# Kernel tuning notes

Hardware: AMD Instinct MI355X
Metric: run time of the kernel (lower is better)

## Reference

```python
import jax, jax.numpy as jnp
import numpy as np

HEADS = 8  # head_num from init_kwargs


def setup_inputs() -> dict:
    key = jax.random.key(0)
    k1, k2, k3 = jax.random.split(key, 3)
    x = jax.random.normal(k1, (1, 512, 16, 16, 16), dtype=jnp.float32)
    # 1x1x1 Conv3d kernels are pointwise linear maps over channels
    w_qkv = jax.random.normal(k2, (1536, 512), dtype=jnp.float32) * 0.02
    w_out = jax.random.normal(k3, (512, 512), dtype=jnp.float32) * 0.02
    return {"x": x, "w_qkv": w_qkv, "w_out": w_out}


def reference(x, w_qkv, w_out):
    B, C, D, H, W = x.shape
    h = HEADS
    dh = C // h
    scale = float(dh) ** 0.5  # NOTE: source MULTIPLIES by sqrt(dh) (dk), faithful here
    N = D * H * W

    # pointwise Conv3d == per-token linear: [B, N, C]
    xt = x.reshape(B, C, N).transpose(0, 2, 1)
    qkv = xt @ w_qkv.T                                   # [B, N, 3C]
    qkv = qkv.reshape(B, N, 3, h, dh).transpose(2, 0, 3, 1, 4)  # [3, B, h, N, dh]
    q, k, v = qkv[0], qkv[1], qkv[2]

    energy = jnp.einsum('bhid,bhjd->bhij', q, k) * scale  # [B, h, N, N]
    attn = jax.nn.softmax(energy, axis=-1)
    o = jnp.einsum('bhij,bhjd->bhid', attn, v)            # [B, h, N, dh]

    o = o.transpose(0, 2, 1, 3).reshape(B, N, C)          # [B, N, C]
    out = o @ w_out.T                                     # [B, N, C]
    return out.transpose(0, 2, 1).reshape(B, C, D, H, W)
```

## Files before the change

### kernel.cpp

```cpp
#include <hip/hip_runtime.h>

typedef unsigned short u16;
typedef unsigned int u32;
typedef unsigned long long u64;
typedef __bf16 bf16x8 __attribute__((ext_vector_type(8)));
typedef float f32x4 __attribute__((ext_vector_type(4)));
typedef u16 u16x8 __attribute__((ext_vector_type(8)));

#define C_DIM 512
#define N_TOK 4096
#define HEADS 8
#define K3 1536
#define QSCALE 11.5415603071f

__device__ __forceinline__ u16 f2bf(float f) {
  u32 u = __builtin_bit_cast(u32, f);
  u += 0x7FFFu + ((u >> 16) & 1u);
  return (u16)(u >> 16);
}
__device__ __forceinline__ float bf2f(u16 b) {
  u32 u = ((u32)b) << 16;
  return __builtin_bit_cast(float, u);
}

__global__ void prep_w_kernel(const float* __restrict__ w, u16* __restrict__ A1) {
  int i = blockIdx.x * 256 + threadIdx.x;
  if (i >= 1536 * 512) return;
  int m = i >> 9, c = i & 511;
  float v = w[i];
  u16 hi = f2bf(v);
  u16 lo = f2bf(v - bf2f(hi));
  u16* row = A1 + (size_t)m * K3;
  row[c] = hi; row[512 + c] = hi; row[1024 + c] = lo;
}

__global__ void prep_wout_kernel(const float* __restrict__ w, u16* __restrict__ A2) {
  int i = blockIdx.x * 256 + threadIdx.x;
  if (i >= 512 * 512) return;
  A2[i] = f2bf(w[i]);
}

__global__ __launch_bounds__(256) void prep_x_kernel(const float* __restrict__ x, u16* __restrict__ B1) {
  __shared__ float lds[64][65];
  int n0 = blockIdx.x * 64, c0 = blockIdx.y * 64;
  int tid = threadIdx.x;
#pragma unroll
  for (int i = 0; i < 4; i++) {
    int idx = tid + i * 256;
    int r = idx >> 4, s = idx & 15;
    const float4 v = *(const float4*)(x + (size_t)(c0 + r) * N_TOK + n0 + s * 4);
    lds[r][s * 4 + 0] = v.x; lds[r][s * 4 + 1] = v.y;
    lds[r][s * 4 + 2] = v.z; lds[r][s * 4 + 3] = v.w;
  }
  __syncthreads();
  int n = tid >> 2, cs = tid & 3;
  u16x8 hv[2], lv[2];
#pragma unroll
  for (int half = 0; half < 2; half++) {
#pragma unroll
    for (int j = 0; j < 8; j++) {
      float v = lds[cs * 16 + half * 8 + j][n];
      u16 hi = f2bf(v);
      hv[half][j] = hi;
      lv[half][j] = f2bf(v - bf2f(hi));
    }
  }
  u16* row = B1 + (size_t)(n0 + n) * K3 + c0 + cs * 16;
  *(u16x8*)(row) = hv[0];
  *(u16x8*)(row + 8) = hv[1];
  *(u16x8*)(row + 512) = lv[0];
  *(u16x8*)(row + 520) = lv[1];
  *(u16x8*)(row + 1024) = hv[0];
  *(u16x8*)(row + 1032) = hv[1];
}

__global__ __launch_bounds__(256) void gemm_nt_kernel(
    const u16* __restrict__ A, const u16* __restrict__ B, float* __restrict__ C,
    int M, int N, int K) {
  __shared__ char lds[128 * 64 * 2 * 2];
  char* ldsA = lds;
  char* ldsB = lds + 128 * 64 * 2;
  int n0 = blockIdx.x * 128, m0 = blockIdx.y * 128;
  int tid = threadIdx.x, lane = tid & 63, wid = tid >> 6;
  int wr = wid >> 1, wc = wid & 1;
  f32x4 acc[4][4] = {};
  for (int k0 = 0; k0 < K; k0 += 64) {
    __syncthreads();
#pragma unroll
    for (int i = 0; i < 4; i++) {
      int idx = tid + i * 256;
      int row = idx >> 3, cb = idx & 7;
      uint4 va = *(const uint4*)(A + (size_t)(m0 + row) * K + k0 + cb * 8);
      *(uint4*)(ldsA + row * 128 + ((cb * 16) ^ ((row & 7) << 4))) = va;
      uint4 vb = *(const uint4*)(B + (size_t)(n0 + row) * K + k0 + cb * 8);
      *(uint4*)(ldsB + row * 128 + ((cb * 16) ^ ((row & 7) << 4))) = vb;
    }
    __syncthreads();
#pragma unroll
    for (int kk = 0; kk < 2; kk++) {
      bf16x8 af[4], bfr[4];
#pragma unroll
      for (int mt = 0; mt < 4; mt++) {
        int row = wr * 64 + mt * 16 + (lane & 15);
        int kb = kk * 64 + ((lane >> 4) << 4);
        af[mt] = *(const bf16x8*)(ldsA + row * 128 + (kb ^ ((row & 7) << 4)));
      }
#pragma unroll
      for (int nt = 0; nt < 4; nt++) {
        int row = wc * 64 + nt * 16 + (lane & 15);
        int kb = kk * 64 + ((lane >> 4) << 4);
        bfr[nt] = *(const bf16x8*)(ldsB + row * 128 + (kb ^ ((row & 7) << 4)));
      }
#pragma unroll
      for (int mt = 0; mt < 4; mt++)
#pragma unroll
        for (int nt = 0; nt < 4; nt++)
          acc[mt][nt] = __builtin_amdgcn_mfma_f32_16x16x32_bf16(af[mt], bfr[nt], acc[mt][nt], 0, 0, 0);
    }
  }
#pragma unroll
  for (int mt = 0; mt < 4; mt++)
#pragma unroll
    for (int nt = 0; nt < 4; nt++) {
      int row = m0 + wr * 64 + mt * 16 + ((lane >> 4) << 2);
      int col = n0 + wc * 64 + nt * 16 + (lane & 15);
#pragma unroll
      for (int r = 0; r < 4; r++)
        C[(size_t)(row + r) * N + col] = acc[mt][nt][r];
    }
}

__global__ void prep_qk_kernel(const float* __restrict__ qkv, u16* __restrict__ Qp, u16* __restrict__ Kp) {
  int i = blockIdx.x * 256 + threadIdx.x;
  int dh = i & 63;
  int n = (i >> 6) & 4095;
  int h = i >> 18;
  float q = qkv[(size_t)n * K3 + h * 64 + dh] * QSCALE;
  float k = qkv[(size_t)n * K3 + 512 + h * 64 + dh];
  u16 qhi = f2bf(q); u16 qlo = f2bf(q - bf2f(qhi));
  u16 khi = f2bf(k); u16 klo = f2bf(k - bf2f(khi));
  u16* qr = Qp + ((size_t)h * N_TOK + n) * 128;
  u16* kr = Kp + ((size_t)h * N_TOK + n) * 128;
  qr[dh] = qhi; qr[64 + dh] = qlo;
  kr[dh] = khi; kr[64 + dh] = klo;
}

__global__ __launch_bounds__(256) void prep_v_kernel(const float* __restrict__ qkv, u16* __restrict__ Vt) {
  __shared__ float lds[64][65];
  int n0 = blockIdx.x * 64, h = blockIdx.y;
  int tid = threadIdx.x;
#pragma unroll
  for (int i = 0; i < 4; i++) {
    int idx = tid + i * 256;
    int r = idx >> 4, s = idx & 15;
    const float4 v = *(const float4*)(qkv + (size_t)(n0 + r) * K3 + 1024 + h * 64 + s * 4);
    lds[r][s * 4 + 0] = v.x; lds[r][s * 4 + 1] = v.y;
    lds[r][s * 4 + 2] = v.z; lds[r][s * 4 + 3] = v.w;
  }
  __syncthreads();
  int dh = tid >> 2, ns = tid & 3;
  u16x8 pv[2];
#pragma unroll
  for (int half = 0; half < 2; half++)
#pragma unroll
    for (int j = 0; j < 8; j++)
      pv[half][j] = f2bf(lds[ns * 16 + half * 8 + j][dh]);
  u16* dst = Vt + ((size_t)h * 64 + dh) * N_TOK + n0 + ns * 16;
  *(u16x8*)(dst) = pv[0];
  *(u16x8*)(dst + 8) = pv[1];
}

__global__ __launch_bounds__(256) void attn_kernel(
    const u16* __restrict__ Qp, const u16* __restrict__ Kp,
    const u16* __restrict__ Vt, float* __restrict__ Uws,
    float* __restrict__ Mws, float* __restrict__ Lws) {
  __shared__ char lds[32768];
  char* ldsK = lds;
  char* ldsV = lds + 16384;
  char* ldsP = lds + 24576;
  int bid = blockIdx.x;
  int h = bid & 7;
  int rest = bid >> 3;
  int half = rest & 1;
  int q0 = (rest >> 1) * 64;
  int kvbase = half * 2048;
  int tid = threadIdx.x, lane = tid & 63, wid = tid >> 6;
  char* myP = ldsP + wid * 2048;
  int qcol = lane & 15;
  int g = lane >> 4;

  bf16x8 qf[4];
  {
    const u16* qrow = Qp + ((size_t)h * N_TOK + q0 + wid * 16 + qcol) * 128 + (g * 8);
#pragma unroll
    for (int c = 0; c < 4; c++) qf[c] = *(const bf16x8*)(qrow + c * 32);
  }
  const u16* Kbase = Kp + (size_t)h * N_TOK * 128;
  const u16* Vbase = Vt + (size_t)h * 64 * N_TOK;

  f32x4 o[4] = {};
  float mrow = -INFINITY, lrow = 0.f;

  for (int t = 0; t < 32; ++t) {
    int kv0 = kvbase + t * 64;
    __syncthreads();
#pragma unroll
    for (int i = 0; i < 4; i++) {
      int idx = tid + i * 256, row = idx >> 4, cb = idx & 15;
      uint4 v = *(const uint4*)(Kbase + (size_t)(kv0 + row) * 128 + cb * 8);
      *(uint4*)(ldsK + row * 256 + ((cb * 16) ^ ((row & 7) << 4))) = v;
    }
#pragma unroll
    for (int i = 0; i < 2; i++) {
      int idx = tid + i * 256, row = idx >> 3, cb = idx & 7;
      uint4 v = *(const uint4*)(Vbase + (size_t)row * N_TOK + kv0 + cb * 8);
      *(uint4*)(ldsV + row * 128 + ((cb * 16) ^ ((row & 7) << 4))) = v;
    }
    __syncthreads();

    f32x4 s[4];
#pragma unroll
    for (int nt = 0; nt < 4; nt++) {
      int row = nt * 16 + qcol;
      const char* kb = ldsK + row * 256;
      int swz = (row & 7) << 4;
      int ko = g << 4;
      bf16x8 kf0 = *(const bf16x8*)(kb + ((ko) ^ swz));
      bf16x8 kf1 = *(const bf16x8*)(kb + ((64 + ko) ^ swz));
      bf16x8 kf2 = *(const bf16x8*)(kb + ((128 + ko) ^ swz));
      bf16x8 kf3 = *(const bf16x8*)(kb + ((192 + ko) ^ swz));
      f32x4 acc = {};
      acc = __builtin_amdgcn_mfma_f32_16x16x32_bf16(kf0, qf[0], acc, 0, 0, 0);
      acc = __builtin_amdgcn_mfma_f32_16x16x32_bf16(kf1, qf[1], acc, 0, 0, 0);
      acc = __builtin_amdgcn_mfma_f32_16x16x32_bf16(kf2, qf[0], acc, 0, 0, 0);
      acc = __builtin_amdgcn_mfma_f32_16x16x32_bf16(kf3, qf[1], acc, 0, 0, 0);
      acc = __builtin_amdgcn_mfma_f32_16x16x32_bf16(kf0, qf[2], acc, 0, 0, 0);
      acc = __builtin_amdgcn_mfma_f32_16x16x32_bf16(kf1, qf[3], acc, 0, 0, 0);
      s[nt] = acc;
    }

    float m = s[0][0];
#pragma unroll
    for (int nt = 0; nt < 4; nt++)
#pragma unroll
      for (int r = 0; r < 4; r++) m = fmaxf(m, s[nt][r]);
    m = fmaxf(m, __shfl_xor(m, 16));
    m = fmaxf(m, __shfl_xor(m, 32));
    float mnew = fmaxf(mrow, m);
    float alpha = exp2f(mrow - mnew);
    mrow = mnew;
    float psum = 0.f;
#pragma unroll
    for (int nt = 0; nt < 4; nt++)
#pragma unroll
      for (int r = 0; r < 4; r++) {
        float p = exp2f(s[nt][r] - mnew);
        s[nt][r] = p;
        psum += p;
      }
    psum += __shfl_xor(psum, 16);
    psum += __shfl_xor(psum, 32);
    lrow = lrow * alpha + psum;

#pragma unroll
    for (int r = 0; r < 4; r++) {
      float a = __shfl(alpha, (g << 2) | r);
      o[0][r] *= a; o[1][r] *= a; o[2][r] *= a; o[3][r] *= a;
    }

#pragma unroll
    for (int nt = 0; nt < 4; nt++) {
      u16 h0 = f2bf(s[nt][0]), h1 = f2bf(s[nt][1]);
      u16 h2 = f2bf(s[nt][2]), h3 = f2bf(s[nt][3]);
      u32 w0 = (u32)h0 | ((u32)h1 << 16);
      u32 w1 = (u32)h2 | ((u32)h3 << 16);
      int off = (nt * 32 + g * 8) ^ ((qcol & 7) << 4);
      *(uint2*)(myP + qcol * 128 + off) = make_uint2(w0, w1);
    }

#pragma unroll
    for (int c = 0; c < 2; c++) {
      int prow = lane & 15;
      int kb2 = c * 64 + (g << 4);
      bf16x8 pf = *(const bf16x8*)(myP + prow * 128 + (kb2 ^ ((prow & 7) << 4)));
#pragma unroll
      for (int nt = 0; nt < 4; nt++) {
        int vrow = nt * 16 + (lane & 15);
        bf16x8 vf = *(const bf16x8*)(ldsV + vrow * 128 + (kb2 ^ ((vrow & 7) << 4)));
        o[nt] = __builtin_amdgcn_mfma_f32_16x16x32_bf16(pf, vf, o[nt], 0, 0, 0);
      }
    }
  }

  size_t base = ((size_t)(half * HEADS + h) * N_TOK);
#pragma unroll
  for (int r = 0; r < 4; r++) {
    int tok = q0 + wid * 16 + (g << 2) + r;
    float* urow = Uws + (base + tok) * 64;
#pragma unroll
    for (int nt = 0; nt < 4; nt++)
      urow[nt * 16 + (lane & 15)] = o[nt][r];
  }
  if (g == 0) {
    int tok = q0 + wid * 16 + qcol;
    Mws[base + tok] = mrow;
    Lws[base + tok] = lrow;
  }
}

__global__ void reduce_kernel(const float* __restrict__ Uws, const float* __restrict__ Mws,
                              const float* __restrict__ Lws, u16* __restrict__ Obuf) {
  int i = blockIdx.x * 256 + threadIdx.x;
  int d4 = i & 15;
  int tok = (i >> 4) & 4095;
  int h = i >> 16;
  size_t b1 = (size_t)h * N_TOK + tok;
  size_t b2 = (size_t)(HEADS + h) * N_TOK + tok;
  float m1 = Mws[b1], m2 = Mws[b2];
  float l1 = Lws[b1], l2 = Lws[b2];
  float m = fmaxf(m1, m2);
  float w1 = exp2f(m1 - m), w2 = exp2f(m2 - m);
  float inv = 1.0f / (l1 * w1 + l2 * w2);
  f32x4 u1 = *(const f32x4*)(Uws + b1 * 64 + d4 * 4);
  f32x4 u2 = *(const f32x4*)(Uws + b2 * 64 + d4 * 4);
  u16* dst = Obuf + (size_t)tok * C_DIM + h * 64 + d4 * 4;
#pragma unroll
  for (int j = 0; j < 4; j++)
    dst[j] = f2bf((u1[j] * w1 + u2[j] * w2) * inv);
}

extern "C" void kernel_launch(void* const* d_in, const int* in_sizes, int n_in,
                              void* d_out, int out_size, void* d_ws, size_t ws_size,
                              hipStream_t stream) {
  const float* x = (const float*)d_in[0];
  const float* w_qkv = (const float*)d_in[1];
  const float* w_out = (const float*)d_in[2];
  float* out = (float*)d_out;
  char* ws = (char*)d_ws;
  size_t off = 0;
  size_t off_B1 = off;  off += (size_t)N_TOK * K3 * 2;
  size_t off_A1 = off;  off += (size_t)K3 * K3 * 2;
  size_t off_A2 = off;  off += (size_t)512 * 512 * 2;
  size_t off_qkv = off; off += (size_t)N_TOK * K3 * 4;
  size_t off_Qp = off;  off += (size_t)HEADS * N_TOK * 128 * 2;
  size_t off_Kp = off;  off += (size_t)HEADS * N_TOK * 128 * 2;
  u16* B1 = (u16*)(ws + off_B1);
  u16* A1 = (u16*)(ws + off_A1);
  u16* A2 = (u16*)(ws + off_A2);
  float* qkv = (float*)(ws + off_qkv);
  u16* Qp = (u16*)(ws + off_Qp);
  u16* Kp = (u16*)(ws + off_Kp);
  u16* Vt = (u16*)(ws + off_A1);
  u16* Obuf = (u16*)(ws + off_B1);
  float* Uws = (float*)(ws + off_qkv);
  float* Mws = (float*)(ws + off_qkv + 16777216);
  float* Lws = (float*)(ws + off_qkv + 16777216 + 262144);

  prep_w_kernel<<<(1536 * 512 + 255) / 256, 256, 0, stream>>>(w_qkv, A1);
  prep_wout_kernel<<<(512 * 512 + 255) / 256, 256, 0, stream>>>(w_out, A2);
  prep_x_kernel<<<dim3(64, 8), 256, 0, stream>>>(x, B1);
  gemm_nt_kernel<<<dim3(K3 / 128, N_TOK / 128), 256, 0, stream>>>(B1, A1, qkv, N_TOK, K3, K3);
  prep_qk_kernel<<<(HEADS * N_TOK * 64) / 256, 256, 0, stream>>>(qkv, Qp, Kp);
  prep_v_kernel<<<dim3(64, 8), 256, 0, stream>>>(qkv, Vt);
  attn_kernel<<<1024, 256, 0, stream>>>(Qp, Kp, Vt, Uws, Mws, Lws);
  reduce_kernel<<<(HEADS * N_TOK * 16) / 256, 256, 0, stream>>>(Uws, Mws, Lws, Obuf);
  gemm_nt_kernel<<<dim3(N_TOK / 128, 512 / 128), 256, 0, stream>>>(A2, Obuf, out, 512, N_TOK, 512);
}
```

Baseline: 235.5 us.

## Pre-swizzle K/V tiles and double-buffer attention loads via global_load_lds

The prep kernels now write K and V into pre-swizzled per-tile images that match the attention kernel's LDS layout. This lets the attention kernel copy tiles straight from global memory into LDS with global_load_lds, bypassing registers. K/V tiles are double-buffered so the next tile's load overlaps current compute, cutting one barrier per iteration. LDS offsets are precomputed and s_setprio is raised around MFMA blocks; the costs are more LDS per block (lower occupancy) and scattered 2-byte writes in prep_qk.

Result: slower. 255.4 us (+8.5%).

```diff
diff --git a/kernel.cpp b/kernel.cpp
--- a/kernel.cpp
+++ b/kernel.cpp
@@ -12,6 +12,11 @@
 #define HEADS 8
 #define K3 1536
 #define QSCALE 11.5415603071f
+
+#define GLDS(SRC, DST)                                                        \
+  __builtin_amdgcn_global_load_lds(                                           \
+      (const __attribute__((address_space(1))) void*)(SRC),                   \
+      (__attribute__((address_space(3))) void*)(DST), 16, 0, 0)
 
 __device__ __forceinline__ u16 f2bf(float f) {
   u32 u = __builtin_bit_cast(u32, f);
@@ -56,13 +61,13 @@
   int n = tid >> 2, cs = tid & 3;
   u16x8 hv[2], lv[2];
 #pragma unroll
-  for (int half = 0; half < 2; half++) {
+  for (int half2 = 0; half2 < 2; half2++) {
 #pragma unroll
     for (int j = 0; j < 8; j++) {
-      float v = lds[cs * 16 + half * 8 + j][n];
+      float v = lds[cs * 16 + half2 * 8 + j][n];
       u16 hi = f2bf(v);
-      hv[half][j] = hi;
-      lv[half][j] = f2bf(v - bf2f(hi));
+      hv[half2][j] = hi;
+      lv[half2][j] = f2bf(v - bf2f(hi));
     }
   }
   u16* row = B1 + (size_t)(n0 + n) * K3 + c0 + cs * 16;
@@ -130,7 +135,7 @@
     }
 }
 
-__global__ void prep_qk_kernel(const float* __restrict__ qkv, u16* __restrict__ Qp, u16* __restrict__ Kp) {
+__global__ void prep_qk_kernel(const float* __restrict__ qkv, u16* __restrict__ Qp, u16* __restrict__ Kimg) {
   int i = blockIdx.x * 256 + threadIdx.x;
   int dh = i & 63;
   int n = (i >> 6) & 4095;
@@ -140,14 +145,20 @@
   u16 qhi = f2bf(q); u16 qlo = f2bf(q - bf2f(qhi));
   u16 khi = f2bf(k); u16 klo = f2bf(k - bf2f(khi));
   u16* qr = Qp + ((size_t)h * N_TOK + n) * 128;
-  u16* kr = Kp + ((size_t)h * N_TOK + n) * 128;
   qr[dh] = qhi; qr[64 + dh] = qlo;
-  kr[dh] = khi; kr[64 + dh] = klo;
-}
-
-__global__ __launch_bounds__(256) void prep_v_kernel(const float* __restrict__ qkv, u16* __restrict__ Vt) {
+  u16* kt = Kimg + ((size_t)h * 64 + (n >> 6)) * 8192;
+  int row = n & 63;
+  int swz = (row & 7) << 4;
+  int bh = row * 256 + (((dh >> 3) * 16) ^ swz);
+  int bl = row * 256 + ((((dh >> 3) + 8) * 16) ^ swz);
+  kt[(bh >> 1) + (dh & 7)] = khi;
+  kt[(bl >> 1) + (dh & 7)] = klo;
+}
+
+__global__ __launch_bounds__(256) void prep_v_kernel(const float* __restrict__ qkv, u16* __restrict__ Vimg) {
   __shared__ float lds[64][65];
-  int n0 = blockIdx.x * 64, h = blockIdx.y;
+  int tile = blockIdx.x, h = blockIdx.y;
+  int n0 = tile * 64;
   int tid = threadIdx.x;
 #pragma unroll
   for (int i = 0; i < 4; i++) {
@@ -159,33 +170,31 @@
   }
   __syncthreads();
   int dh = tid >> 2, ns = tid & 3;
-  u16x8 pv[2];
-#pragma unroll
-  for (int half = 0; half < 2; half++)
+  u16* vt = Vimg + ((size_t)h * 64 + tile) * 4096;
+#pragma unroll
+  for (int half2 = 0; half2 < 2; half2++) {
+    u16x8 pv;
 #pragma unroll
     for (int j = 0; j < 8; j++)
-      pv[half][j] = f2bf(lds[ns * 16 + half * 8 + j][dh]);
-  u16* dst = Vt + ((size_t)h * 64 + dh) * N_TOK + n0 + ns * 16;
-  *(u16x8*)(dst) = pv[0];
-  *(u16x8*)(dst + 8) = pv[1];
+      pv[j] = f2bf(lds[ns * 16 + half2 * 8 + j][dh]);
+    int cb = ns * 2 + half2;
+    int off = dh * 64 + ((((cb * 16) ^ ((dh & 7) << 4))) >> 1);
+    *(u16x8*)(vt + off) = pv;
+  }
 }
 
 __global__ __launch_bounds__(256) void attn_kernel(
-    const u16* __restrict__ Qp, const u16* __restrict__ Kp,
-    const u16* __restrict__ Vt, float* __restrict__ Uws,
+    const u16* __restrict__ Qp, const u16* __restrict__ Kimg,
+    const u16* __restrict__ Vimg, float* __restrict__ Uws,
     float* __restrict__ Mws, float* __restrict__ Lws) {
-  __shared__ char lds[32768];
-  char* ldsK = lds;
-  char* ldsV = lds + 16384;
-  char* ldsP = lds + 24576;
+  __shared__ char lds[57344];
   int bid = blockIdx.x;
   int h = bid & 7;
   int rest = bid >> 3;
   int half = rest & 1;
   int q0 = (rest >> 1) * 64;
-  int kvbase = half * 2048;
   int tid = threadIdx.x, lane = tid & 63, wid = tid >> 6;
-  char* myP = ldsP + wid * 2048;
+  char* myP = lds + 49152 + wid * 2048;
   int qcol = lane & 15;
   int g = lane >> 4;
 
@@ -195,40 +204,63 @@
 #pragma unroll
     for (int c = 0; c < 4; c++) qf[c] = *(const bf16x8*)(qrow + c * 32);
   }
-  const u16* Kbase = Kp + (size_t)h * N_TOK * 128;
-  const u16* Vbase = Vt + (size_t)h * 64 * N_TOK;
+
+  const char* ksrc = (const char*)Kimg + ((size_t)h * 64 + half * 32) * 16384 + wid * 1024 + lane * 16;
+  const char* vsrc = (const char*)Vimg + ((size_t)h * 64 + half * 32) * 8192 + wid * 1024 + lane * 16;
+
+  int koff[4][4];
+  int voff[2][4];
+  int poffw[4], poffr[2];
+#pragma unroll
+  for (int nt = 0; nt < 4; nt++) {
+    int row = nt * 16 + qcol;
+    int swz = (row & 7) << 4;
+#pragma unroll
+    for (int c = 0; c < 4; c++)
+      koff[nt][c] = row * 256 + ((c * 64 + g * 16) ^ swz);
+    int vrow = nt * 16 + qcol;
+    int vswz = (vrow & 7) << 4;
+#pragma unroll
+    for (int c = 0; c < 2; c++)
+      voff[c][nt] = vrow * 128 + ((c * 64 + g * 16) ^ vswz);
+    poffw[nt] = qcol * 128 + ((nt * 32 + g * 8) ^ ((qcol & 7) << 4));
+  }
+#pragma unroll
+  for (int c = 0; c < 2; c++)
+    poffr[c] = qcol * 128 + ((c * 64 + g * 16) ^ ((qcol & 7) << 4));
+
+#pragma unroll
+  for (int j = 0; j < 4; j++) GLDS(ksrc + j * 4096, lds + wid * 1024 + j * 4096);
+#pragma unroll
+  for (int j = 0; j < 2; j++) GLDS(vsrc + j * 4096, lds + 32768 + wid * 1024 + j * 4096);
+  __syncthreads();
 
   f32x4 o[4] = {};
   float mrow = -INFINITY, lrow = 0.f;
+  int cur = 0;
 
   for (int t = 0; t < 32; ++t) {
-    int kv0 = kvbase + t * 64;
-    __syncthreads();
-#pragma unroll
-    for (int i = 0; i < 4; i++) {
-      int idx = tid + i * 256, row = idx >> 4, cb = idx & 15;
-      uint4 v = *(const uint4*)(Kbase + (size_t)(kv0 + row) * 128 + cb * 8);
-      *(uint4*)(ldsK + row * 256 + ((cb * 16) ^ ((row & 7) << 4))) = v;
-    }
-#pragma unroll
-    for (int i = 0; i < 2; i++) {
-      int idx = tid + i * 256, row = idx >> 3, cb = idx & 7;
-      uint4 v = *(const uint4*)(Vbase + (size_t)row * N_TOK + kv0 + cb * 8);
-      *(uint4*)(ldsV + row * 128 + ((cb * 16) ^ ((row & 7) << 4))) = v;
-    }
-    __syncthreads();
+    if (t < 31) {
+      const char* kn = ksrc + (size_t)(t + 1) * 16384;
+      const char* vn = vsrc + (size_t)(t + 1) * 8192;
+      char* kd = lds + (cur ^ 1) * 16384 + wid * 1024;
+      char* vd = lds + 32768 + (cur ^ 1) * 8192 + wid * 1024;
+#pragma unroll
+      for (int j = 0; j < 4; j++) GLDS(kn + j * 4096, kd + j * 4096);
+#pragma unroll
+      for (int j = 0; j < 2; j++) GLDS(vn + j * 4096, vd + j * 4096);
+    }
+    const char* kbuf = lds + cur * 16384;
+    const char* vbuf = lds + 32768 + cur * 8192;
 
     f32x4 s[4];
+    __builtin_amdgcn_s_setprio(1);
 #pragma unroll
     for (int nt = 0; nt < 4; nt++) {
-      int row = nt * 16 + qcol;
-      const char* kb = ldsK + row * 256;
-      int swz = (row & 7) << 4;
-      int ko = g << 4;
-      bf16x8 kf0 = *(const bf16x8*)(kb + ((ko) ^ swz));
-      bf16x8 kf1 = *(const bf16x8*)(kb + ((64 + ko) ^ swz));
-      bf16x8 kf2 = *(const bf16x8*)(kb + ((128 + ko) ^ swz));
-      bf16x8 kf3 = *(const bf16x8*)(kb + ((192 + ko) ^ swz));
+      bf16x8 kf0 = *(const bf16x8*)(kbuf + koff[nt][0]);
+      bf16x8 kf1 = *(const bf16x8*)(kbuf + koff[nt][1]);
+      bf16x8 kf2 = *(const bf16x8*)(kbuf + koff[nt][2]);
+      bf16x8 kf3 = *(const bf16x8*)(kbuf + koff[nt][3]);
       f32x4 acc = {};
       acc = __builtin_amdgcn_mfma_f32_16x16x32_bf16(kf0, qf[0], acc, 0, 0, 0);
       acc = __builtin_amdgcn_mfma_f32_16x16x32_bf16(kf1, qf[1], acc, 0, 0, 0);
@@ -238,6 +270,7 @@
       acc = __builtin_amdgcn_mfma_f32_16x16x32_bf16(kf1, qf[3], acc, 0, 0, 0);
       s[nt] = acc;
     }
+    __builtin_amdgcn_s_setprio(0);
 
     float m = s[0][0];
 #pragma unroll
@@ -274,22 +307,23 @@
       u16 h2 = f2bf(s[nt][2]), h3 = f2bf(s[nt][3]);
       u32 w0 = (u32)h0 | ((u32)h1 << 16);
       u32 w1 = (u32)h2 | ((u32)h3 << 16);
-      int off = (nt * 32 + g * 8) ^ ((qcol & 7) << 4);
-      *(uint2*)(myP + qcol * 128 + off) = make_uint2(w0, w1);
-    }
-
+      *(uint2*)(myP + poffw[nt]) = make_uint2(w0, w1);
+    }
+
+    __builtin_amdgcn_s_setprio(1);
 #pragma unroll
     for (int c = 0; c < 2; c++) {
-      int prow = lane & 15;
-      int kb2 = c * 64 + (g << 4);
-      bf16x8 pf = *(const bf16x8*)(myP + prow * 128 + (kb2 ^ ((prow & 7) << 4)));
+      bf16x8 pf = *(const bf16x8*)(myP + poffr[c]);
 #pragma unroll
       for (int nt = 0; nt < 4; nt++) {
-        int vrow = nt * 16 + (lane & 15);
-        bf16x8 vf = *(const bf16x8*)(ldsV + vrow * 128 + (kb2 ^ ((vrow & 7) << 4)));
+        bf16x8 vf = *(const bf16x8*)(vbuf + voff[c][nt]);
         o[nt] = __builtin_amdgcn_mfma_f32_16x16x32_bf16(pf, vf, o[nt], 0, 0, 0);
       }
     }
+    __builtin_amdgcn_s_setprio(0);
+
+    __syncthreads();
+    cur ^= 1;
   }
 
   size_t base = ((size_t)(half * HEADS + h) * N_TOK);
@@ -349,8 +383,8 @@
   u16* A2 = (u16*)(ws + off_A2);
   float* qkv = (float*)(ws + off_qkv);
   u16* Qp = (u16*)(ws + off_Qp);
-  u16* Kp = (u16*)(ws + off_Kp);
-  u16* Vt = (u16*)(ws + off_A1);
+  u16* Kimg = (u16*)(ws + off_Kp);
+  u16* Vimg = (u16*)(ws + off_A1);
   u16* Obuf = (u16*)(ws + off_B1);
   float* Uws = (float*)(ws + off_qkv);
   float* Mws = (float*)(ws + off_qkv + 16777216);
@@ -360,9 +394,9 @@
   prep_wout_kernel<<<(512 * 512 + 255) / 256, 256, 0, stream>>>(w_out, A2);
   prep_x_kernel<<<dim3(64, 8), 256, 0, stream>>>(x, B1);
   gemm_nt_kernel<<<dim3(K3 / 128, N_TOK / 128), 256, 0, stream>>>(B1, A1, qkv, N_TOK, K3, K3);
-  prep_qk_kernel<<<(HEADS * N_TOK * 64) / 256, 256, 0, stream>>>(qkv, Qp, Kp);
-  prep_v_kernel<<<dim3(64, 8), 256, 0, stream>>>(qkv, Vt);
-  attn_kernel<<<1024, 256, 0, stream>>>(Qp, Kp, Vt, Uws, Mws, Lws);
+  prep_qk_kernel<<<(HEADS * N_TOK * 64) / 256, 256, 0, stream>>>(qkv, Qp, Kimg);
+  prep_v_kernel<<<dim3(64, 8), 256, 0, stream>>>(qkv, Vimg);
+  attn_kernel<<<1024, 256, 0, stream>>>(Qp, Kimg, Vimg, Uws, Mws, Lws);
   reduce_kernel<<<(HEADS * N_TOK * 16) / 256, 256, 0, stream>>>(Uws, Mws, Lws, Obuf);
   gemm_nt_kernel<<<dim3(N_TOK / 128, 512 / 128), 256, 0, stream>>>(A2, Obuf, out, 512, N_TOK, 512);
 }
```
